# Optimization experiments

Measured on AMD Instinct MI355X. Metric: run time of the kernel, lower is better.

## Reference

```python
import jax, jax.numpy as jnp
import numpy as np
from jax import lax

FEAT_STRIDE = 16
RATIOS = np.array([0.5, 1.0, 2.0], np.float32)
SCALES = np.array([8.0, 16.0, 32.0], np.float32)
A = RATIOS.size * SCALES.size            # 9 anchors per location
N_PRE = 3000                             # pre-NMS top-k (TEST-style config)
N_POST = 300                             # post-NMS rois per image
NMS_THRESH = 0.7
MIN_SIZE = 16.0
B, C, HF, WF = 4, 512, 50, 50


def setup_inputs() -> dict:
    key = jax.random.key(0)
    ks = jax.random.split(key, 4)
    mid = 512
    return {
        "inputs": jax.random.normal(ks[0], (B, C, HF, WF), jnp.float32),
        "conv_w": jax.random.normal(ks[1], (mid, C, 3, 3), jnp.float32) * 0.01,
        "conv_b": jnp.zeros((mid,), jnp.float32),
        "bf_w": jax.random.normal(ks[2], (A * 2, mid, 1, 1), jnp.float32) * 0.01,
        "bf_b": jnp.zeros((A * 2,), jnp.float32),
        "loc_w": jax.random.normal(ks[3], (A * 4, mid, 1, 1), jnp.float32) * 0.01,
        "loc_b": jnp.zeros((A * 4,), jnp.float32),
        "img_h": 800,
        "img_w": 800,
    }


def _conv(x, w, b, pad):
    y = lax.conv_general_dilated(x, w, (1, 1), [(pad, pad), (pad, pad)],
                                 dimension_numbers=("NCHW", "OIHW", "NCHW"))
    return y + b[None, :, None, None]


def _anchors(hf, wf):
    ratios = jnp.asarray(RATIOS)
    scales = jnp.asarray(SCALES)
    hs = (FEAT_STRIDE * scales[None, :] * jnp.sqrt(ratios[:, None])).reshape(-1)
    ws = (FEAT_STRIDE * scales[None, :] * jnp.sqrt(1.0 / ratios[:, None])).reshape(-1)
    c = FEAT_STRIDE / 2.0
    base = jnp.stack([c - hs / 2, c - ws / 2, c + hs / 2, c + ws / 2], 1)  # [A,4] yxyx
    sy = jnp.arange(hf, dtype=jnp.float32) * FEAT_STRIDE
    sx = jnp.arange(wf, dtype=jnp.float32) * FEAT_STRIDE
    yy, xx = jnp.meshgrid(sy, sx, indexing="ij")
    shifts = jnp.stack([yy, xx, yy, xx], -1).reshape(-1, 1, 4)
    return (shifts + base[None]).reshape(-1, 4)  # [hf*wf*A, 4]


def _decode(anchors, loc):
    # anchors [N,4] yxyx, loc [B,N,4] (dy,dx,dh,dw)
    ah = anchors[:, 2] - anchors[:, 0]
    aw = anchors[:, 3] - anchors[:, 1]
    acy = anchors[:, 0] + 0.5 * ah
    acx = anchors[:, 1] + 0.5 * aw
    cy = loc[..., 0] * ah + acy
    cx = loc[..., 1] * aw + acx
    h = jnp.exp(loc[..., 2]) * ah
    w = jnp.exp(loc[..., 3]) * aw
    return jnp.stack([cy - 0.5 * h, cx - 0.5 * w, cy + 0.5 * h, cx + 0.5 * w], -1)


def _nms(boxes, scores):
    # boxes [N,4], scores [N] -> fixed-size [N_POST,4] rois (zero-padded)
    hs = boxes[:, 2] - boxes[:, 0]
    ws = boxes[:, 3] - boxes[:, 1]
    valid = (hs >= MIN_SIZE) & (ws >= MIN_SIZE)
    s = jnp.where(valid, scores, -jnp.inf)
    order = jnp.argsort(-s)[:N_PRE]
    b = boxes[order]
    v = valid[order]
    sb = lax.stop_gradient(b)
    area = (sb[:, 2] - sb[:, 0]) * (sb[:, 3] - sb[:, 1])
    tl = jnp.maximum(sb[:, None, :2], sb[None, :, :2])
    br = jnp.minimum(sb[:, None, 2:], sb[None, :, 2:])
    wh = jnp.clip(br - tl, 0.0)
    inter = wh[..., 0] * wh[..., 1]
    iou = inter / (area[:, None] + area[None, :] - inter + 1e-9)

    def body(i, keep):
        sup = jnp.any((iou[i] > NMS_THRESH) & keep)
        return keep.at[i].set(v[i] & ~sup)

    keep = lax.fori_loop(0, N_PRE, body, jnp.zeros((N_PRE,), bool))
    pos = jnp.where(keep, jnp.cumsum(keep) - 1, N_POST)  # invalid -> dropped
    return jnp.zeros((N_POST, 4), boxes.dtype).at[pos].set(b, mode="drop")


def reference(inputs, conv_w, conv_b, bf_w, bf_b, loc_w, loc_b, img_h, img_w):
    b_, _, hf, wf = inputs.shape
    feat = jax.nn.relu(_conv(inputs, conv_w, conv_b, 1))
    loc = _conv(feat, loc_w, loc_b, 0).transpose(0, 2, 3, 1).reshape(b_, -1, 4)
    logits = _conv(feat, bf_w, bf_b, 0).transpose(0, 2, 3, 1).reshape(b_, hf, wf, A, 2)
    probs = jax.nn.softmax(logits, axis=4)
    fg = probs[..., 1].reshape(b_, -1)             # foreground scores [B, hf*wf*A]
    bf_pred = probs.reshape(b_, -1, 2)
    anchors = _anchors(hf, wf)
    boxes = _decode(anchors, loc)
    boxes = jnp.stack([
        jnp.clip(boxes[..., 0], 0.0, img_h), jnp.clip(boxes[..., 1], 0.0, img_w),
        jnp.clip(boxes[..., 2], 0.0, img_h), jnp.clip(boxes[..., 3], 0.0, img_w)], -1)
    rois = jax.vmap(_nms)(boxes, fg).reshape(-1, 4)         # [B*N_POST, 4]
    rois_idx = jnp.repeat(jnp.arange(b_, dtype=jnp.int32), N_POST)
    return rois, rois_idx, anchors, loc, bf_pred
```

## Files before the change

kernel.cpp:

```cpp
#include <hip/hip_runtime.h>
#include <hip/hip_bf16.h>
#include <math.h>

#define BIMG   4
#define CIN    512
#define MID    512
#define HF     50
#define WF     50
#define PIX    2500
#define MTOT   10000
#define ANC    9
#define NLOC   22500
#define NPRE   3000
#define NPOST  300
#define WORDS  47
#define ROWPAD 3008
#define WSTRIDE 48
#define CAP    8192

#define ROIS_OFF 0
#define IDX_OFF  4800
#define ANC_OFF  6000
#define LOC_OFF  96000
#define BF_OFF   456000

#define WS_WT     0UL
#define WS_W1T    9437184UL
#define WS_FEAT   9568256UL
#define WS_SCORE  30048256UL
#define WS_BOXD   30768256UL
#define WS_SBD    33648256UL
#define WS_M      34032256UL
#define WS_CAND   38652544UL
#define WS_CNT    38783616UL
#define WS_PART1  38786048UL
#define WS_PART2  59266048UL
#define WS_PART3  79746048UL
#define WS_NEED2  59266048UL
#define WS_NEED4  100226048UL

__global__ __launch_bounds__(256) void prep_kernel(
    const float* __restrict__ conv_w, const float* __restrict__ loc_w,
    const float* __restrict__ bf_w, float* __restrict__ Wt, float* __restrict__ W1t) {
  int o = blockIdx.x * 256 + threadIdx.x;
  if (o < 4608 * 512) {
    int co  = o & 511;
    int k   = o >> 9;
    int c   = k & 511;
    int tap = k >> 9;
    Wt[o] = conv_w[(co * 512 + c) * 9 + tap];
  } else {
    int o2 = o - 4608 * 512;
    if (o2 < 512 * 64) {
      int co = o2 & 63;
      int c  = o2 >> 6;
      float v = 0.0f;
      if (co < 36)      v = loc_w[co * 512 + c];
      else if (co < 54) v = bf_w[(co - 36) * 512 + c];
      W1t[o2] = v;
    }
  }
}

__device__ __forceinline__ void stage_load(
    int kb, int sg, bool in0, bool in1,
    int y0, int x0, int y1, int x1,
    const float* __restrict__ ib0, const float* __restrict__ ib1, float av[8]) {
  int tap = kb >> 5;
  int c0  = (kb & 31) << 4;
  int t3  = tap / 3;
  int dy  = t3 - 1;
  int dx  = tap - t3 * 3 - 1;
  int iy0 = y0 + dy, ix0 = x0 + dx;
  int iy1 = y1 + dy, ix1 = x1 + dx;
  bool ok0 = in0 && ((unsigned)iy0 < (unsigned)HF) && ((unsigned)ix0 < (unsigned)WF);
  bool ok1 = in1 && ((unsigned)iy1 < (unsigned)HF) && ((unsigned)ix1 < (unsigned)WF);
  int base = (c0 + sg * 4) * PIX;
  int o0 = iy0 * WF + ix0;
  int o1 = iy1 * WF + ix1;
#pragma unroll
  for (int j = 0; j < 4; ++j) {
    av[2 * j]     = ok0 ? ib0[base + j * PIX + o0] : 0.0f;
    av[2 * j + 1] = ok1 ? ib1[base + j * PIX + o1] : 0.0f;
  }
}

__global__ __launch_bounds__(256, 3) void conv3x3_kernel(
    const float* __restrict__ in, const float* __restrict__ Wt,
    float* __restrict__ part0, float* __restrict__ part1,
    float* __restrict__ part2, float* __restrict__ part3) {
  __shared__ float As[2][16][128];
  const int tid = threadIdx.x;
  const int q0 = blockIdx.x * 128;
  const int lane = tid & 63;
  const int wv = tid >> 6;
  const int col0 = __builtin_amdgcn_readfirstlane(blockIdx.y * 64 + wv * 16);
  const int half = 288 / gridDim.z;
  const int kb0 = blockIdx.z * half;
  float* __restrict__ dst = (blockIdx.z == 0) ? part0 :
                            (blockIdx.z == 1) ? part1 :
                            (blockIdx.z == 2) ? part2 : part3;

  const int sg = tid >> 6;
  const int sp = tid & 63;
  int qs0 = q0 + 2 * sp, qs1 = qs0 + 1;
  bool in0 = qs0 < MTOT, in1 = qs1 < MTOT;
  int t0 = in0 ? qs0 : 0, t1 = in1 ? qs1 : 0;
  int b0i = t0 / PIX, r0 = t0 - b0i * PIX, y0 = r0 / WF, x0 = r0 - y0 * WF;
  int b1i = t1 / PIX, r1 = t1 - b1i * PIX, y1 = r1 / WF, x1 = r1 - y1 * WF;
  const float* ib0 = in + (size_t)b0i * (CIN * PIX);
  const float* ib1 = in + (size_t)b1i * (CIN * PIX);

  double acc[2][16];
  float accf[2][16];
#pragma unroll
  for (int p = 0; p < 2; ++p)
#pragma unroll
    for (int c = 0; c < 16; ++c) { acc[p][c] = 0.0; accf[p][c] = 0.0f; }

  {
    float av[8];
    stage_load(kb0, sg, in0, in1, y0, x0, y1, x1, ib0, ib1, av);
#pragma unroll
    for (int j = 0; j < 4; ++j)
      *(float2*)&As[0][sg * 4 + j][2 * sp] = make_float2(av[2 * j], av[2 * j + 1]);
  }
  __syncthreads();

  for (int kbl = 0; kbl < half; ++kbl) {
    int kb = kb0 + kbl;
    int cur = kbl & 1;
    float av[8];
    bool has_next = (kbl + 1 < half);
    if (has_next)
      stage_load(kb + 1, sg, in0, in1, y0, x0, y1, x1, ib0, ib1, av);

    const float* __restrict__ Bw = Wt + (size_t)(kb * 16) * 512 + col0;
#pragma unroll
    for (int kg = 0; kg < 4; ++kg) {
#pragma unroll
      for (int kq = 0; kq < 4; ++kq) {
        int kk = kg * 4 + kq;
        const float* __restrict__ br = Bw + (size_t)kk * 512;
        float2 a = *(const float2*)&As[cur][kk][2 * lane];
#pragma unroll
        for (int c = 0; c < 16; ++c) {
          float bv = br[c];
          accf[0][c] = fmaf(a.x, bv, accf[0][c]);
          accf[1][c] = fmaf(a.y, bv, accf[1][c]);
        }
      }
    }
    if (kbl & 1) {
#pragma unroll
      for (int p = 0; p < 2; ++p)
#pragma unroll
        for (int c = 0; c < 16; ++c) {
          acc[p][c] += (double)accf[p][c];
          accf[p][c] = 0.0f;
        }
    }
    if (has_next) {
      int nxt = cur ^ 1;
#pragma unroll
      for (int j = 0; j < 4; ++j)
        *(float2*)&As[nxt][sg * 4 + j][2 * sp] = make_float2(av[2 * j], av[2 * j + 1]);
    }
    __syncthreads();
  }

#pragma unroll
  for (int p = 0; p < 2; ++p) {
    int q = q0 + 2 * lane + p;
    if (q < MTOT) {
      float o[16];
#pragma unroll
      for (int c = 0; c < 16; ++c) o[c] = (float)acc[p][c];
      float* fp = &dst[(size_t)q * 512 + col0];
#pragma unroll
      for (int g = 0; g < 4; ++g)
        *(float4*)&fp[g * 4] = make_float4(o[g*4], o[g*4+1], o[g*4+2], o[g*4+3]);
    }
  }
}

__global__ __launch_bounds__(256) void conv1x1_kernel(
    const float* __restrict__ p0, const float* __restrict__ p1,
    const float* __restrict__ p2, const float* __restrict__ p3, int nz,
    const float* __restrict__ convb, const float* __restrict__ W1t,
    const float* __restrict__ locb, const float* __restrict__ bfb,
    double* __restrict__ rawd) {
  __shared__ float As[16][128];
  const int tid = threadIdx.x;
  const int q0 = blockIdx.x * 128;
  const int lane = tid & 63;
  const int wv = tid >> 6;
  const int col0 = __builtin_amdgcn_readfirstlane(wv * 16);

  const int pixL = tid >> 1;
  const int ch   = (tid & 1) * 8;
  const int qL   = q0 + pixL;
  const bool okL = qL < MTOT;

  double acc[2][16];
  float accf[2][16];
#pragma unroll
  for (int p = 0; p < 2; ++p)
#pragma unroll
    for (int c = 0; c < 16; ++c) { acc[p][c] = 0.0; accf[p][c] = 0.0f; }

  for (int kb = 0; kb < 32; ++kb) {
    int c0 = kb * 16;
    float fv[8];
#pragma unroll
    for (int k = 0; k < 8; ++k) fv[k] = 0.0f;
    if (okL) {
      const size_t base = (size_t)qL * 512 + c0 + ch;
      double s[8];
      float4 a0 = *(const float4*)&p0[base];
      float4 a1 = *(const float4*)&p0[base + 4];
      s[0] = (double)a0.x; s[1] = (double)a0.y; s[2] = (double)a0.z; s[3] = (double)a0.w;
      s[4] = (double)a1.x; s[5] = (double)a1.y; s[6] = (double)a1.z; s[7] = (double)a1.w;
      if (nz > 1) {
        float4 b0 = *(const float4*)&p1[base];
        float4 b1 = *(const float4*)&p1[base + 4];
        s[0] += (double)b0.x; s[1] += (double)b0.y; s[2] += (double)b0.z; s[3] += (double)b0.w;
        s[4] += (double)b1.x; s[5] += (double)b1.y; s[6] += (double)b1.z; s[7] += (double)b1.w;
      }
      if (nz > 2) {
        float4 c0v = *(const float4*)&p2[base];
        float4 c1v = *(const float4*)&p2[base + 4];
        s[0] += (double)c0v.x; s[1] += (double)c0v.y; s[2] += (double)c0v.z; s[3] += (double)c0v.w;
        s[4] += (double)c1v.x; s[5] += (double)c1v.y; s[6] += (double)c1v.z; s[7] += (double)c1v.w;
        float4 d0 = *(const float4*)&p3[base];
        float4 d1 = *(const float4*)&p3[base + 4];
        s[0] += (double)d0.x; s[1] += (double)d0.y; s[2] += (double)d0.z; s[3] += (double)d0.w;
        s[4] += (double)d1.x; s[5] += (double)d1.y; s[6] += (double)d1.z; s[7] += (double)d1.w;
      }
      float4 bs0 = *(const float4*)&convb[c0 + ch];
      float4 bs1 = *(const float4*)&convb[c0 + ch + 4];
      fv[0] = (float)fmax(s[0] + (double)bs0.x, 0.0);
      fv[1] = (float)fmax(s[1] + (double)bs0.y, 0.0);
      fv[2] = (float)fmax(s[2] + (double)bs0.z, 0.0);
      fv[3] = (float)fmax(s[3] + (double)bs0.w, 0.0);
      fv[4] = (float)fmax(s[4] + (double)bs1.x, 0.0);
      fv[5] = (float)fmax(s[5] + (double)bs1.y, 0.0);
      fv[6] = (float)fmax(s[6] + (double)bs1.z, 0.0);
      fv[7] = (float)fmax(s[7] + (double)bs1.w, 0.0);
    }
    __syncthreads();
#pragma unroll
    for (int k = 0; k < 8; ++k) As[ch + k][pixL] = fv[k];
    __syncthreads();

    const float* __restrict__ Bw = W1t + (size_t)c0 * 64 + col0;
#pragma unroll
    for (int kk = 0; kk < 16; ++kk) {
      const float* __restrict__ br = Bw + (size_t)kk * 64;
      float2 a = *(const float2*)&As[kk][2 * lane];
#pragma unroll
      for (int c = 0; c < 16; ++c) {
        float bv = br[c];
        accf[0][c] = fmaf(a.x, bv, accf[0][c]);
        accf[1][c] = fmaf(a.y, bv, accf[1][c]);
      }
    }
    if (kb & 1) {
#pragma unroll
      for (int p = 0; p < 2; ++p)
#pragma unroll
        for (int c = 0; c < 16; ++c) {
          acc[p][c] += (double)accf[p][c];
          accf[p][c] = 0.0f;
        }
    }
  }

  double bs[16];
#pragma unroll
  for (int c = 0; c < 16; ++c) {
    int co = col0 + c;
    bs[c] = (co < 36) ? (double)locb[co] : ((co < 54) ? (double)bfb[co - 36] : 0.0);
  }
#pragma unroll
  for (int p = 0; p < 2; ++p) {
    int q = q0 + 2 * lane + p;
    if (q < MTOT) {
      double* rp = &rawd[(size_t)q * 64 + col0];
#pragma unroll
      for (int c = 0; c < 16; ++c) rp[c] = acc[p][c] + bs[c];
    }
  }
}

__global__ __launch_bounds__(256) void epilogue_kernel(
    const double* __restrict__ rawd, float* __restrict__ d_out,
    double* __restrict__ boxd, unsigned long long* __restrict__ ukey,
    const int* __restrict__ imh, const int* __restrict__ imw) {
  int idx = blockIdx.x * 256 + threadIdx.x;
  if (idx >= BIMG * NLOC) return;
  int b = idx / NLOC;
  int i = idx - b * NLOC;
  int p = i / ANC;
  int a = i - p * ANC;
  int y = p / WF;
  int x = p - y * WF;
  int q = b * PIX + p;

  double l0d = rawd[(size_t)q * 64 + a * 4 + 0];
  double l1d = rawd[(size_t)q * 64 + a * 4 + 1];
  double l2d = rawd[(size_t)q * 64 + a * 4 + 2];
  double l3d = rawd[(size_t)q * 64 + a * 4 + 3];
  float4 lo = make_float4((float)l0d, (float)l1d, (float)l2d, (float)l3d);
  *(float4*)&d_out[LOC_OFF + (size_t)idx * 4] = lo;

  double g0 = rawd[(size_t)q * 64 + 36 + a * 2];
  double g1 = rawd[(size_t)q * 64 + 37 + a * 2];
  double m  = fmax(g0, g1);
  double e0 = exp(g0 - m), e1 = exp(g1 - m);
  double s  = e0 + e1;
  double p0 = e0 / s, p1 = e1 / s;
  *(float2*)&d_out[BF_OFF + (size_t)idx * 2] = make_float2((float)p0, (float)p1);

  int ridx = a / 3, sidx = a - ridx * 3;
  double ratio = (ridx == 0) ? 0.5 : ((ridx == 1) ? 1.0 : 2.0);
  double scale = (sidx == 0) ? 8.0 : ((sidx == 1) ? 16.0 : 32.0);
  double hs = 16.0 * scale * sqrt(ratio);
  double ws = 16.0 * scale * sqrt(1.0 / ratio);
  double sy = (double)(y * 16), sx = (double)(x * 16);
  double a0 = sy + (8.0 - hs * 0.5);
  double a1 = sx + (8.0 - ws * 0.5);
  double a2 = sy + (8.0 + hs * 0.5);
  double a3 = sx + (8.0 + ws * 0.5);
  if (b == 0) {
    *(float4*)&d_out[ANC_OFF + (size_t)i * 4] =
        make_float4((float)a0, (float)a1, (float)a2, (float)a3);
  }

  double ah = a2 - a0, aw = a3 - a1;
  double acy = a0 + 0.5 * ah, acx = a1 + 0.5 * aw;
  double cy = l0d * ah + acy;
  double cx = l1d * aw + acx;
  double hh = exp(l2d) * ah;
  double ww = exp(l3d) * aw;
  double ihf = (double)imh[0], iwf = (double)imw[0];
  double b0 = fmin(fmax(cy - 0.5 * hh, 0.0), ihf);
  double b1 = fmin(fmax(cx - 0.5 * ww, 0.0), iwf);
  double b2 = fmin(fmax(cy + 0.5 * hh, 0.0), ihf);
  double b3 = fmin(fmax(cx + 0.5 * ww, 0.0), iwf);
  double* bp = &boxd[(size_t)idx * 4];
  bp[0] = b0; bp[1] = b1; bp[2] = b2; bp[3] = b3;

  bool valid = (b2 - b0 >= 16.0) && (b3 - b1 >= 16.0);
  double d = valid ? (g1 - g0) : -INFINITY;
  long long bits = __double_as_longlong(d);
  unsigned long long u = (bits < 0)
      ? ~(unsigned long long)bits
      : ((unsigned long long)bits | 0x8000000000000000ull);
  ukey[idx] = ~u;
}

__global__ __launch_bounds__(1024) void thresh_kernel(
    const unsigned long long* __restrict__ ukey,
    unsigned* __restrict__ ccnt, unsigned* __restrict__ cand) {
  __shared__ unsigned hist[16384];
  __shared__ unsigned csum[1024];
  __shared__ unsigned sT, scnt;
  int b = blockIdx.x;
  int tid = threadIdx.x;
  for (int i = tid; i < 16384; i += 1024) hist[i] = 0;
  if (tid == 0) scnt = 0;
  __syncthreads();
  for (int j = tid; j < NLOC; j += 1024)
    atomicAdd(&hist[(unsigned)(ukey[(size_t)b * NLOC + j] >> 50)], 1u);
  __syncthreads();
  unsigned s = 0;
#pragma unroll
  for (int k = 0; k < 16; ++k) s += hist[tid * 16 + k];
  csum[tid] = s;
  __syncthreads();
  if (tid == 0) {
    unsigned cum = 0;
    int T = 16383;
    for (int c = 0; c < 1024; ++c) {
      if (cum + csum[c] >= NPRE) {
        unsigned cc = cum;
        for (int k = 0; k < 16; ++k) {
          cc += hist[c * 16 + k];
          if (cc >= NPRE) { T = c * 16 + k; break; }
        }
        break;
      }
      cum += csum[c];
    }
    sT = (unsigned)T;
  }
  __syncthreads();
  unsigned T = sT;
  for (int j = tid; j < NLOC; j += 1024) {
    if ((unsigned)(ukey[(size_t)b * NLOC + j] >> 50) <= T) {
      unsigned slot = atomicAdd(&scnt, 1u);
      if (slot < CAP) cand[(size_t)b * CAP + slot] = (unsigned)j;
    }
  }
  __syncthreads();
  if (tid == 0) ccnt[b] = scnt;
}

__global__ __launch_bounds__(256) void rank_kernel(
    const unsigned long long* __restrict__ ukey, const unsigned* __restrict__ ccnt,
    const unsigned* __restrict__ cand, const double* __restrict__ boxd,
    double* __restrict__ sbd) {
  __shared__ unsigned long long kt[256];
  __shared__ unsigned it[256];
  int b = blockIdx.y;
  int C = (int)min(ccnt[b], (unsigned)CAP);
  int s = blockIdx.x * 256 + threadIdx.x;
  bool act = s < C;
  unsigned myi = act ? cand[(size_t)b * CAP + s] : 0xFFFFFFFFu;
  unsigned long long ki = act ? ukey[(size_t)b * NLOC + myi] : ~0ull;
  int cnt = 0;
  int ntile = (C + 255) >> 8;
  for (int t = 0; t < ntile; ++t) {
    int j = t * 256 + threadIdx.x;
    unsigned ji = (j < C) ? cand[(size_t)b * CAP + j] : 0xFFFFFFFFu;
    kt[threadIdx.x] = (j < C) ? ukey[(size_t)b * NLOC + ji] : ~0ull;
    it[threadIdx.x] = ji;
    __syncthreads();
#pragma unroll 8
    for (int jj = 0; jj < 256; ++jj) {
      unsigned long long kj = kt[jj];
      unsigned jidx = it[jj];
      cnt += ((kj < ki) || (kj == ki && jidx < myi)) ? 1 : 0;
    }
    __syncthreads();
  }
  if (act && cnt < NPRE) {
    const double* bx = &boxd[((size_t)b * NLOC + myi) * 4];
    double* dp = &sbd[((size_t)b * NPRE + cnt) * 4];
    dp[0] = bx[0]; dp[1] = bx[1]; dp[2] = bx[2]; dp[3] = bx[3];
  }
}

__global__ __launch_bounds__(64) void nmsmask_kernel(
    const double* __restrict__ sbd, unsigned long long* __restrict__ M) {
  __shared__ double cb[64][4];
  int b = blockIdx.z;
  int jw = blockIdx.y;
  int i  = blockIdx.x * 64 + threadIdx.x;
  int j  = jw * 64 + threadIdx.x;
  double j0 = 0, j1 = 0, j2 = 0, j3 = 0;
  if (j < NPRE) {
    const double* bp = &sbd[((size_t)b * NPRE + j) * 4];
    j0 = bp[0]; j1 = bp[1]; j2 = bp[2]; j3 = bp[3];
  }
  cb[threadIdx.x][0] = j0; cb[threadIdx.x][1] = j1;
  cb[threadIdx.x][2] = j2; cb[threadIdx.x][3] = j3;
  __syncthreads();
  if (i >= NPRE) return;
  const double* bp = &sbd[((size_t)b * NPRE + i) * 4];
  double i0 = bp[0], i1 = bp[1], i2 = bp[2], i3 = bp[3];
  double ai = (i2 - i0) * (i3 - i1);
  unsigned long long mask = 0ull;
#pragma unroll 4
  for (int t = 0; t < 64; ++t) {
    double aj = (cb[t][2] - cb[t][0]) * (cb[t][3] - cb[t][1]);
    double h = fmax(fmin(i2, cb[t][2]) - fmax(i0, cb[t][0]), 0.0);
    double w = fmax(fmin(i3, cb[t][3]) - fmax(i1, cb[t][1]), 0.0);
    double inter = h * w;
    double iou = inter / (ai + aj - inter + 1e-9);
    mask |= ((iou > 0.7) ? 1ull : 0ull) << t;
  }
  M[((size_t)b * ROWPAD + i) * WSTRIDE + jw] = mask;
}

__global__ __launch_bounds__(64) void nms_scan_kernel(
    const double* __restrict__ sbd, const unsigned long long* __restrict__ M,
    float* __restrict__ d_out) {
  int b = blockIdx.x;
  int lane = threadIdx.x;
  for (int k = lane; k < NPOST; k += 64) {
    *(float4*)&d_out[ROIS_OFF + (size_t)(b * NPOST + k) * 4] = make_float4(0, 0, 0, 0);
    d_out[IDX_OFF + b * NPOST + k] = (float)b;
  }
  __syncthreads();

  unsigned long long R = ~0ull;
  if (lane < WORDS) R = 0ull;
  for (int w = 0; w < WORDS; ++w) {
    int j = w * 64 + lane;
    bool inval = true;
    if (j < NPRE) {
      const double* bp = &sbd[((size_t)b * NPRE + j) * 4];
      double h = bp[2] - bp[0], wd = bp[3] - bp[1];
      inval = !(h >= 16.0 && wd >= 16.0);
    }
    unsigned long long bal = __ballot(inval ? 1 : 0);
    if (lane == w) R |= bal;
  }

  int kept = 0;
  while (kept < NPOST) {
    unsigned long long hz = __ballot(((~R) != 0ull) ? 1 : 0);
    if (hz == 0ull) break;
    int w0 = __ffsll(hz) - 1;
    unsigned long long word = __shfl(R, w0);
    int bit = __ffsll(~word) - 1;
    int i = w0 * 64 + bit;
    if (lane < 4)
      d_out[ROIS_OFF + (size_t)(b * NPOST + kept) * 4 + lane] =
          (float)sbd[((size_t)b * NPRE + i) * 4 + lane];
    kept++;
    if (kept >= NPOST) break;
    unsigned long long row = (lane < WORDS)
        ? M[((size_t)b * ROWPAD + i) * WSTRIDE + lane] : 0ull;
    R |= row;
    if (lane == w0) R |= (1ull << bit);
  }
}

extern "C" void kernel_launch(void* const* d_in, const int* in_sizes, int n_in,
                              void* d_out, int out_size, void* d_ws, size_t ws_size,
                              hipStream_t stream) {
  const float* in     = (const float*)d_in[0];
  const float* conv_w = (const float*)d_in[1];
  const float* conv_b = (const float*)d_in[2];
  const float* bf_w   = (const float*)d_in[3];
  const float* bf_b   = (const float*)d_in[4];
  const float* loc_w  = (const float*)d_in[5];
  const float* loc_b  = (const float*)d_in[6];
  const int*   imh    = (const int*)d_in[7];
  const int*   imw    = (const int*)d_in[8];
  float* out = (float*)d_out;

  char* ws = (char*)d_ws;
  float*  Wt    = (float*)(ws + WS_WT);
  double* rawd  = (double*)(ws + WS_WT);
  float*  W1t   = (float*)(ws + WS_W1T);
  float*  part0 = (float*)(ws + WS_FEAT);
  unsigned long long* ukey = (unsigned long long*)(ws + WS_SCORE);
  double* boxd  = (double*)(ws + WS_BOXD);
  double* sbd   = (double*)(ws + WS_SBD);
  unsigned long long* M = (unsigned long long*)(ws + WS_M);
  unsigned* cand = (unsigned*)(ws + WS_CAND);
  unsigned* ccnt = (unsigned*)(ws + WS_CNT);
  float*  part1 = (float*)(ws + WS_PART1);
  float*  part2 = (float*)(ws + WS_PART2);
  float*  part3 = (float*)(ws + WS_PART3);

  const int nz = (ws_size >= WS_NEED4) ? 4 : ((ws_size >= WS_NEED2) ? 2 : 1);

  hipLaunchKernelGGL(prep_kernel, dim3((4608 * 512 + 512 * 64 + 255) / 256), dim3(256),
                     0, stream, conv_w, loc_w, bf_w, Wt, W1t);
  hipLaunchKernelGGL(conv3x3_kernel, dim3(79, 8, nz), dim3(256), 0, stream,
                     in, Wt, part0, part1, part2, part3);
  hipLaunchKernelGGL(conv1x1_kernel, dim3(79), dim3(256), 0, stream,
                     part0, part1, part2, part3, nz, conv_b, W1t, loc_b, bf_b, rawd);
  hipLaunchKernelGGL(epilogue_kernel, dim3((BIMG * NLOC + 255) / 256), dim3(256), 0, stream,
                     rawd, out, boxd, ukey, imh, imw);
  hipLaunchKernelGGL(thresh_kernel, dim3(4), dim3(1024), 0, stream, ukey, ccnt, cand);
  hipLaunchKernelGGL(rank_kernel, dim3(CAP / 256, 4), dim3(256), 0, stream,
                     ukey, ccnt, cand, boxd, sbd);
  hipLaunchKernelGGL(nmsmask_kernel, dim3(47, 47, 4), dim3(64), 0, stream, sbd, M);
  hipLaunchKernelGGL(nms_scan_kernel, dim3(4), dim3(64), 0, stream, sbd, M, out);
}
```

Baseline: 1.387 ms.

## Split 1x1 conv over K into four partial outputs and pack 3x3 FMAs

```diff
diff --git a/kernel.cpp b/kernel.cpp
--- a/kernel.cpp
+++ b/kernel.cpp
@@ -1,6 +1,8 @@
 #include <hip/hip_runtime.h>
 #include <hip/hip_bf16.h>
 #include <math.h>
+
+typedef float v2f __attribute__((ext_vector_type(2)));
 
 #define BIMG   4
 #define CIN    512
@@ -38,6 +40,7 @@
 #define WS_PART3  79746048UL
 #define WS_NEED2  59266048UL
 #define WS_NEED4  100226048UL
+#define RAWP_SZ   2560000UL
 
 __global__ __launch_bounds__(256) void prep_kernel(
     const float* __restrict__ conv_w, const float* __restrict__ loc_w,
@@ -112,11 +115,12 @@
   const float* ib1 = in + (size_t)b1i * (CIN * PIX);
 
   double acc[2][16];
-  float accf[2][16];
-#pragma unroll
-  for (int p = 0; p < 2; ++p)
-#pragma unroll
-    for (int c = 0; c < 16; ++c) { acc[p][c] = 0.0; accf[p][c] = 0.0f; }
+  v2f accf2[16];
+  const v2f vzero = {0.0f, 0.0f};
+#pragma unroll
+  for (int c = 0; c < 16; ++c) {
+    acc[0][c] = 0.0; acc[1][c] = 0.0; accf2[c] = vzero;
+  }
 
   {
     float av[8];
@@ -142,23 +146,22 @@
       for (int kq = 0; kq < 4; ++kq) {
         int kk = kg * 4 + kq;
         const float* __restrict__ br = Bw + (size_t)kk * 512;
-        float2 a = *(const float2*)&As[cur][kk][2 * lane];
+        v2f a2 = *(const v2f*)&As[cur][kk][2 * lane];
 #pragma unroll
         for (int c = 0; c < 16; ++c) {
           float bv = br[c];
-          accf[0][c] = fmaf(a.x, bv, accf[0][c]);
-          accf[1][c] = fmaf(a.y, bv, accf[1][c]);
+          v2f b2 = {bv, bv};
+          accf2[c] = __builtin_elementwise_fma(a2, b2, accf2[c]);
         }
       }
     }
     if (kbl & 1) {
 #pragma unroll
-      for (int p = 0; p < 2; ++p)
-#pragma unroll
-        for (int c = 0; c < 16; ++c) {
-          acc[p][c] += (double)accf[p][c];
-          accf[p][c] = 0.0f;
-        }
+      for (int c = 0; c < 16; ++c) {
+        acc[0][c] += (double)accf2[c][0];
+        acc[1][c] += (double)accf2[c][1];
+        accf2[c] = vzero;
+      }
     }
     if (has_next) {
       int nxt = cur ^ 1;
@@ -188,114 +191,94 @@
     const float* __restrict__ p0, const float* __restrict__ p1,
     const float* __restrict__ p2, const float* __restrict__ p3, int nz,
     const float* __restrict__ convb, const float* __restrict__ W1t,
-    const float* __restrict__ locb, const float* __restrict__ bfb,
-    double* __restrict__ rawd) {
-  __shared__ float As[16][128];
+    float* __restrict__ rawp0, float* __restrict__ rawp1,
+    float* __restrict__ rawp2, float* __restrict__ rawp3) {
+  __shared__ float As[16][64];
   const int tid = threadIdx.x;
-  const int q0 = blockIdx.x * 128;
+  const int q0 = blockIdx.x * 64;
+  const int by = blockIdx.y;
   const int lane = tid & 63;
   const int wv = tid >> 6;
   const int col0 = __builtin_amdgcn_readfirstlane(wv * 16);
-
-  const int pixL = tid >> 1;
-  const int ch   = (tid & 1) * 8;
-  const int qL   = q0 + pixL;
-  const bool okL = qL < MTOT;
-
-  double acc[2][16];
-  float accf[2][16];
-#pragma unroll
-  for (int p = 0; p < 2; ++p)
-#pragma unroll
-    for (int c = 0; c < 16; ++c) { acc[p][c] = 0.0; accf[p][c] = 0.0f; }
-
-  for (int kb = 0; kb < 32; ++kb) {
+  float* __restrict__ rp = (by == 0) ? rawp0 : (by == 1) ? rawp1 :
+                           (by == 2) ? rawp2 : rawp3;
+
+  const int sg = tid >> 6;
+  const int sp = tid & 63;
+  const int qs = q0 + sp;
+  const bool okL = qs < MTOT;
+
+  double acc[16];
+  float accf[16];
+#pragma unroll
+  for (int c = 0; c < 16; ++c) { acc[c] = 0.0; accf[c] = 0.0f; }
+
+  for (int kbl = 0; kbl < 8; ++kbl) {
+    int kb = by * 8 + kbl;
     int c0 = kb * 16;
-    float fv[8];
-#pragma unroll
-    for (int k = 0; k < 8; ++k) fv[k] = 0.0f;
+    float fv[4] = {0.0f, 0.0f, 0.0f, 0.0f};
     if (okL) {
-      const size_t base = (size_t)qL * 512 + c0 + ch;
-      double s[8];
+      const size_t base = (size_t)qs * 512 + c0 + sg * 4;
+      double s[4];
       float4 a0 = *(const float4*)&p0[base];
-      float4 a1 = *(const float4*)&p0[base + 4];
       s[0] = (double)a0.x; s[1] = (double)a0.y; s[2] = (double)a0.z; s[3] = (double)a0.w;
-      s[4] = (double)a1.x; s[5] = (double)a1.y; s[6] = (double)a1.z; s[7] = (double)a1.w;
       if (nz > 1) {
         float4 b0 = *(const float4*)&p1[base];
-        float4 b1 = *(const float4*)&p1[base + 4];
         s[0] += (double)b0.x; s[1] += (double)b0.y; s[2] += (double)b0.z; s[3] += (double)b0.w;
-        s[4] += (double)b1.x; s[5] += (double)b1.y; s[6] += (double)b1.z; s[7] += (double)b1.w;
       }
       if (nz > 2) {
         float4 c0v = *(const float4*)&p2[base];
-        float4 c1v = *(const float4*)&p2[base + 4];
         s[0] += (double)c0v.x; s[1] += (double)c0v.y; s[2] += (double)c0v.z; s[3] += (double)c0v.w;
-        s[4] += (double)c1v.x; s[5] += (double)c1v.y; s[6] += (double)c1v.z; s[7] += (double)c1v.w;
         float4 d0 = *(const float4*)&p3[base];
-        float4 d1 = *(const float4*)&p3[base + 4];
         s[0] += (double)d0.x; s[1] += (double)d0.y; s[2] += (double)d0.z; s[3] += (double)d0.w;
-        s[4] += (double)d1.x; s[5] += (double)d1.y; s[6] += (double)d1.z; s[7] += (double)d1.w;
       }
-      float4 bs0 = *(const float4*)&convb[c0 + ch];
-      float4 bs1 = *(const float4*)&convb[c0 + ch + 4];
-      fv[0] = (float)fmax(s[0] + (double)bs0.x, 0.0);
-      fv[1] = (float)fmax(s[1] + (double)bs0.y, 0.0);
-      fv[2] = (float)fmax(s[2] + (double)bs0.z, 0.0);
-      fv[3] = (float)fmax(s[3] + (double)bs0.w, 0.0);
-      fv[4] = (float)fmax(s[4] + (double)bs1.x, 0.0);
-      fv[5] = (float)fmax(s[5] + (double)bs1.y, 0.0);
-      fv[6] = (float)fmax(s[6] + (double)bs1.z, 0.0);
-      fv[7] = (float)fmax(s[7] + (double)bs1.w, 0.0);
+      float4 bsv = *(const float4*)&convb[c0 + sg * 4];
+      fv[0] = (float)fmax(s[0] + (double)bsv.x, 0.0);
+      fv[1] = (float)fmax(s[1] + (double)bsv.y, 0.0);
+      fv[2] = (float)fmax(s[2] + (double)bsv.z, 0.0);
+      fv[3] = (float)fmax(s[3] + (double)bsv.w, 0.0);
     }
     __syncthreads();
 #pragma unroll
-    for (int k = 0; k < 8; ++k) As[ch + k][pixL] = fv[k];
+    for (int j = 0; j < 4; ++j) As[sg * 4 + j][sp] = fv[j];
     __syncthreads();
 
     const float* __restrict__ Bw = W1t + (size_t)c0 * 64 + col0;
 #pragma unroll
     for (int kk = 0; kk < 16; ++kk) {
       const float* __restrict__ br = Bw + (size_t)kk * 64;
-      float2 a = *(const float2*)&As[kk][2 * lane];
+      float a = As[kk][lane];
+#pragma unroll
+      for (int c = 0; c < 16; ++c)
+        accf[c] = fmaf(a, br[c], accf[c]);
+    }
+    if (kbl & 1) {
 #pragma unroll
       for (int c = 0; c < 16; ++c) {
-        float bv = br[c];
-        accf[0][c] = fmaf(a.x, bv, accf[0][c]);
-        accf[1][c] = fmaf(a.y, bv, accf[1][c]);
+        acc[c] += (double)accf[c];
+        accf[c] = 0.0f;
       }
     }
-    if (kb & 1) {
-#pragma unroll
-      for (int p = 0; p < 2; ++p)
-#pragma unroll
-        for (int c = 0; c < 16; ++c) {
-          acc[p][c] += (double)accf[p][c];
-          accf[p][c] = 0.0f;
-        }
-    }
-  }
-
-  double bs[16];
-#pragma unroll
-  for (int c = 0; c < 16; ++c) {
-    int co = col0 + c;
-    bs[c] = (co < 36) ? (double)locb[co] : ((co < 54) ? (double)bfb[co - 36] : 0.0);
-  }
-#pragma unroll
-  for (int p = 0; p < 2; ++p) {
-    int q = q0 + 2 * lane + p;
-    if (q < MTOT) {
-      double* rp = &rawd[(size_t)q * 64 + col0];
-#pragma unroll
-      for (int c = 0; c < 16; ++c) rp[c] = acc[p][c] + bs[c];
-    }
+  }
+
+  int q = q0 + lane;
+  if (q < MTOT) {
+    float o[16];
+#pragma unroll
+    for (int c = 0; c < 16; ++c) o[c] = (float)acc[c];
+    float* fp = &rp[(size_t)q * 64 + col0];
+#pragma unroll
+    for (int g = 0; g < 4; ++g)
+      *(float4*)&fp[g * 4] = make_float4(o[g*4], o[g*4+1], o[g*4+2], o[g*4+3]);
   }
 }
 
 __global__ __launch_bounds__(256) void epilogue_kernel(
-    const double* __restrict__ rawd, float* __restrict__ d_out,
-    double* __restrict__ boxd, unsigned long long* __restrict__ ukey,
+    const float* __restrict__ r0, const float* __restrict__ r1,
+    const float* __restrict__ r2, const float* __restrict__ r3,
+    const float* __restrict__ locb, const float* __restrict__ bfb,
+    float* __restrict__ d_out, double* __restrict__ boxd,
+    unsigned long long* __restrict__ ukey,
     const int* __restrict__ imh, const int* __restrict__ imw) {
   int idx = blockIdx.x * 256 + threadIdx.x;
   if (idx >= BIMG * NLOC) return;
@@ -306,16 +289,25 @@
   int y = p / WF;
   int x = p - y * WF;
   int q = b * PIX + p;
-
-  double l0d = rawd[(size_t)q * 64 + a * 4 + 0];
-  double l1d = rawd[(size_t)q * 64 + a * 4 + 1];
-  double l2d = rawd[(size_t)q * 64 + a * 4 + 2];
-  double l3d = rawd[(size_t)q * 64 + a * 4 + 3];
-  float4 lo = make_float4((float)l0d, (float)l1d, (float)l2d, (float)l3d);
-  *(float4*)&d_out[LOC_OFF + (size_t)idx * 4] = lo;
-
-  double g0 = rawd[(size_t)q * 64 + 36 + a * 2];
-  double g1 = rawd[(size_t)q * 64 + 37 + a * 2];
+  const size_t rb = (size_t)q * 64;
+
+  float4 A0 = *(const float4*)&r0[rb + a * 4];
+  float4 A1 = *(const float4*)&r1[rb + a * 4];
+  float4 A2 = *(const float4*)&r2[rb + a * 4];
+  float4 A3 = *(const float4*)&r3[rb + a * 4];
+  double l0d = (((double)A0.x + (double)A1.x) + (double)A2.x) + (double)A3.x + (double)locb[a * 4 + 0];
+  double l1d = (((double)A0.y + (double)A1.y) + (double)A2.y) + (double)A3.y + (double)locb[a * 4 + 1];
+  double l2d = (((double)A0.z + (double)A1.z) + (double)A2.z) + (double)A3.z + (double)locb[a * 4 + 2];
+  double l3d = (((double)A0.w + (double)A1.w) + (double)A2.w) + (double)A3.w + (double)locb[a * 4 + 3];
+  *(float4*)&d_out[LOC_OFF + (size_t)idx * 4] =
+      make_float4((float)l0d, (float)l1d, (float)l2d, (float)l3d);
+
+  float2 G0 = *(const float2*)&r0[rb + 36 + a * 2];
+  float2 G1 = *(const float2*)&r1[rb + 36 + a * 2];
+  float2 G2 = *(const float2*)&r2[rb + 36 + a * 2];
+  float2 G3 = *(const float2*)&r3[rb + 36 + a * 2];
+  double g0 = (((double)G0.x + (double)G1.x) + (double)G2.x) + (double)G3.x + (double)bfb[a * 2 + 0];
+  double g1 = (((double)G0.y + (double)G1.y) + (double)G2.y) + (double)G3.y + (double)bfb[a * 2 + 1];
   double m  = fmax(g0, g1);
   double e0 = exp(g0 - m), e1 = exp(g1 - m);
   double s  = e0 + e1;
@@ -535,7 +527,6 @@
 
   char* ws = (char*)d_ws;
   float*  Wt    = (float*)(ws + WS_WT);
-  double* rawd  = (double*)(ws + WS_WT);
   float*  W1t   = (float*)(ws + WS_W1T);
   float*  part0 = (float*)(ws + WS_FEAT);
   unsigned long long* ukey = (unsigned long long*)(ws + WS_SCORE);
@@ -547,6 +538,10 @@
   float*  part1 = (float*)(ws + WS_PART1);
   float*  part2 = (float*)(ws + WS_PART2);
   float*  part3 = (float*)(ws + WS_PART3);
+  float*  rawp0 = (float*)(ws + WS_WT);
+  float*  rawp1 = (float*)(ws + WS_WT + RAWP_SZ);
+  float*  rawp2 = (float*)(ws + WS_WT + 2 * RAWP_SZ);
+  float*  rawp3 = (float*)(ws + WS_M);
 
   const int nz = (ws_size >= WS_NEED4) ? 4 : ((ws_size >= WS_NEED2) ? 2 : 1);
 
@@ -554,10 +549,11 @@
                      0, stream, conv_w, loc_w, bf_w, Wt, W1t);
   hipLaunchKernelGGL(conv3x3_kernel, dim3(79, 8, nz), dim3(256), 0, stream,
                      in, Wt, part0, part1, part2, part3);
-  hipLaunchKernelGGL(conv1x1_kernel, dim3(79), dim3(256), 0, stream,
-                     part0, part1, part2, part3, nz, conv_b, W1t, loc_b, bf_b, rawd);
+  hipLaunchKernelGGL(conv1x1_kernel, dim3(157, 4), dim3(256), 0, stream,
+                     part0, part1, part2, part3, nz, conv_b, W1t,
+                     rawp0, rawp1, rawp2, rawp3);
   hipLaunchKernelGGL(epilogue_kernel, dim3((BIMG * NLOC + 255) / 256), dim3(256), 0, stream,
-                     rawd, out, boxd, ukey, imh, imw);
+                     rawp0, rawp1, rawp2, rawp3, loc_b, bf_b, out, boxd, ukey, imh, imw);
   hipLaunchKernelGGL(thresh_kernel, dim3(4), dim3(1024), 0, stream, ukey, ccnt, cand);
   hipLaunchKernelGGL(rank_kernel, dim3(CAP / 256, 4), dim3(256), 0, stream,
                      ukey, ccnt, cand, boxd, sbd);
```

Result: slower. 1.982 ms (+42.9%).
